# Optimization experiments

Measured on AMD Instinct MI355X. Metric: run time of the kernel, lower is better.

Reference implementation:

```python
import jax, jax.numpy as jnp
import numpy as np

B, I, H, O, T = 512, 512, 1024, 512, 128

def setup_inputs() -> dict:
    key = jax.random.key(0)
    ks = jax.random.split(key, 8)
    s_in = 1.0 / np.sqrt(I)
    s_h = 1.0 / np.sqrt(H)
    return {
        "x": jax.random.normal(ks[0], (B, I), dtype=jnp.float32),
        "h0": jnp.zeros((B, H), dtype=jnp.float32),
        "Wjx": jax.random.normal(ks[1], (H, I), dtype=jnp.float32) * s_in,
        "bjx": jnp.zeros((H,), dtype=jnp.float32),
        "Wjh": jax.random.normal(ks[2], (H, H), dtype=jnp.float32) * s_h,
        "bjh": jnp.zeros((H,), dtype=jnp.float32),
        "Wkx": jax.random.normal(ks[3], (H, I), dtype=jnp.float32) * s_in,
        "bkx": jnp.zeros((H,), dtype=jnp.float32),
        "Wkh": jax.random.normal(ks[4], (H, H), dtype=jnp.float32) * s_h,
        "bkh": jnp.zeros((H,), dtype=jnp.float32),
        "Wo": jax.random.normal(ks[5], (O, H), dtype=jnp.float32) * s_h,
        "bo": jnp.zeros((O,), dtype=jnp.float32),
        "seq_length": T,
    }

def reference(x, h0, Wjx, bjx, Wjh, bjh, Wkx, bkx, Wkh, bkh, Wo, bo, seq_length):
    # x is broadcast to every timestep (original repeats x along time).
    # Precompute the time-invariant input projections once; same math.
    jx = x @ Wjx.T + bjx  # [B,H]
    kx = x @ Wkx.T + bkx  # [B,H]

    def step(h, _):
        j = jax.nn.sigmoid(jx + h @ Wjh.T + bjh)
        k = jax.nn.sigmoid(kx + h @ Wkh.T + bkh)
        new_h = j * (1.0 - h) + (1.0 - k) * h
        out = new_h @ Wo.T + bo  # [B,O]
        return new_h, out

    h_final, outs = jax.lax.scan(step, h0, None, length=seq_length)
    outputs = jnp.transpose(outs, (1, 0, 2))  # [B,T,O]
    return outputs, h_final
```

## Files before the change

### kernel.cpp

```cpp
#include <hip/hip_runtime.h>
#include <hip/hip_bf16.h>
#include <hip/hip_cooperative_groups.h>

namespace cg = cooperative_groups;

constexpr int B = 512;
constexpr int I = 512;
constexpr int H = 1024;
constexpr int O = 512;

using short8 = __attribute__((ext_vector_type(8))) short;
using f32x4  = __attribute__((ext_vector_type(4))) float;
using bf16_t = __hip_bfloat16;

__device__ __forceinline__ short8 ldfrag(const bf16_t* p) {
    return *reinterpret_cast<const short8*>(p);
}
__device__ __forceinline__ float sigmoid_f(float z) {
    return 1.0f / (1.0f + __expf(-z));
}

__device__ __forceinline__ void group_wait(int* c, int target) {
    if (threadIdx.x == 0) {
        while (__hip_atomic_load(c, __ATOMIC_RELAXED, __HIP_MEMORY_SCOPE_AGENT) < target)
            __builtin_amdgcn_s_sleep(2);
    }
    __syncthreads();
    asm volatile("buffer_inv sc0" ::: "memory");
}
__device__ __forceinline__ void group_post(int* c) {
    __syncthreads();
    if (threadIdx.x == 0)
        __hip_atomic_fetch_add(c, 1, __ATOMIC_RELAXED, __HIP_MEMORY_SCOPE_AGENT);
}

__global__ __launch_bounds__(256, 2)
void flipflop_rnn_kernel(const float* __restrict__ x,  const float* __restrict__ h0,
                         const float* __restrict__ Wjx, const float* __restrict__ bjx,
                         const float* __restrict__ Wjh, const float* __restrict__ bjh,
                         const float* __restrict__ Wkx, const float* __restrict__ bkx,
                         const float* __restrict__ Wkh, const float* __restrict__ bkh,
                         const float* __restrict__ Wo,  const float* __restrict__ bo,
                         const int* __restrict__ seqlen,
                         float* __restrict__ out,
                         bf16_t* __restrict__ wjh_bf, bf16_t* __restrict__ wkh_bf,
                         bf16_t* __restrict__ wo_bf,  bf16_t* __restrict__ wjx_bf,
                         bf16_t* __restrict__ wkx_bf, bf16_t* __restrict__ x_bf,
                         bf16_t* __restrict__ hbf0,   bf16_t* __restrict__ hbf1,
                         int* __restrict__ cnt)
{
    __shared__ short lds_w[32768];

    const int T    = seqlen[0];
    const int tid  = threadIdx.x;
    const int g    = blockIdx.x;
    const int nthr = gridDim.x * blockDim.x;
    const int gtid = g * blockDim.x + tid;

    for (int idx = gtid; idx < H * H; idx += nthr) wjh_bf[idx] = __float2bfloat16(Wjh[idx]);
    for (int idx = gtid; idx < H * H; idx += nthr) wkh_bf[idx] = __float2bfloat16(Wkh[idx]);
    for (int idx = gtid; idx < O * H; idx += nthr) wo_bf[idx]  = __float2bfloat16(Wo[idx]);
    for (int idx = gtid; idx < H * I; idx += nthr) wjx_bf[idx] = __float2bfloat16(Wjx[idx]);
    for (int idx = gtid; idx < H * I; idx += nthr) wkx_bf[idx] = __float2bfloat16(Wkx[idx]);
    for (int idx = gtid; idx < B * I; idx += nthr) x_bf[idx]   = __float2bfloat16(x[idx]);
    if (gtid < 8 * 256) cnt[gtid] = 0;

    const int w     = tid >> 6;
    const int lane  = tid & 63;
    const int quad  = lane >> 4;
    const int lm    = lane & 15;
    const int iblk  = g & 7;
    const int lblk  = g >> 3;
    const int rbase = iblk * 64 + w * 16;
    const int n0    = lblk * 16;
    const bool has_out = (lblk < 32);
    const int no0   = lblk * 16;
    int* grp_cnt = cnt + iblk * 256;

    float hreg[4];
    #pragma unroll
    for (int r = 0; r < 4; ++r) {
        const int row = rbase + quad * 4 + r;
        const int col = n0 + lm;
        const float hv = h0[row * H + col];
        hreg[r] = hv;
        hbf0[row * H + col] = __float2bfloat16(hv);
    }

    cg::this_grid().sync();

    for (int c = tid; c < 4096; c += 256) {
        const int gate = c >> 11;
        const int cc   = c & 2047;
        const int kb   = cc >> 4;
        const int col  = cc & 15;
        const bf16_t* src = (gate ? wkh_bf : wjh_bf) + (n0 + col) * H + kb * 8;
        *reinterpret_cast<short8*>(&lds_w[c * 8]) = *reinterpret_cast<const short8*>(src);
    }
    __syncthreads();

    float jxr[4], kxr[4];
    {
        f32x4 aJ = {0.f, 0.f, 0.f, 0.f};
        f32x4 aK = {0.f, 0.f, 0.f, 0.f};
        const bf16_t* aP = x_bf   + (rbase + lm) * I + quad * 8;
        const bf16_t* jP = wjx_bf + (n0 + lm) * I + quad * 8;
        const bf16_t* kP = wkx_bf + (n0 + lm) * I + quad * 8;
        #pragma unroll 4
        for (int k0 = 0; k0 < I; k0 += 32) {
            short8 a = ldfrag(aP + k0);
            aJ = __builtin_amdgcn_mfma_f32_16x16x32_bf16(a, ldfrag(jP + k0), aJ, 0, 0, 0);
            aK = __builtin_amdgcn_mfma_f32_16x16x32_bf16(a, ldfrag(kP + k0), aK, 0, 0, 0);
        }
        const int col = n0 + lm;
        #pragma unroll
        for (int r = 0; r < 4; ++r) {
            jxr[r] = aJ[r] + bjx[col] + bjh[col];
            kxr[r] = aK[r] + bkx[col] + bkh[col];
        }
    }
    const float bo_v = has_out ? bo[no0 + lm] : 0.0f;

    for (int t = 0; t < T; ++t) {
        if (t > 0) group_wait(grp_cnt + t, 64);
        const bf16_t* hb  = (t & 1) ? hbf1 : hbf0;
        bf16_t*       hbn = (t & 1) ? hbf0 : hbf1;

        f32x4 accJ = {0.f, 0.f, 0.f, 0.f};
        f32x4 accK = {0.f, 0.f, 0.f, 0.f};
        f32x4 accO = {0.f, 0.f, 0.f, 0.f};

        const bf16_t* aP = hb    + (rbase + lm) * H + quad * 8;
        const bf16_t* oP = wo_bf + (no0 + lm) * H + quad * 8;
        const short*  jL = lds_w + quad * 128 + lm * 8;
        const short*  kL = jL + 16384;

        if (has_out) {
            #pragma unroll 4
            for (int k0 = 0; k0 < H; k0 += 32) {
                short8 a  = ldfrag(aP + k0);
                short8 bj = *reinterpret_cast<const short8*>(jL + (k0 >> 3) * 128);
                short8 bk = *reinterpret_cast<const short8*>(kL + (k0 >> 3) * 128);
                accJ = __builtin_amdgcn_mfma_f32_16x16x32_bf16(a, bj, accJ, 0, 0, 0);
                accK = __builtin_amdgcn_mfma_f32_16x16x32_bf16(a, bk, accK, 0, 0, 0);
                accO = __builtin_amdgcn_mfma_f32_16x16x32_bf16(a, ldfrag(oP + k0), accO, 0, 0, 0);
            }
        } else {
            #pragma unroll 4
            for (int k0 = 0; k0 < H; k0 += 32) {
                short8 a  = ldfrag(aP + k0);
                short8 bj = *reinterpret_cast<const short8*>(jL + (k0 >> 3) * 128);
                short8 bk = *reinterpret_cast<const short8*>(kL + (k0 >> 3) * 128);
                accJ = __builtin_amdgcn_mfma_f32_16x16x32_bf16(a, bj, accJ, 0, 0, 0);
                accK = __builtin_amdgcn_mfma_f32_16x16x32_bf16(a, bk, accK, 0, 0, 0);
            }
        }

        if (has_out && t > 0) {
            #pragma unroll
            for (int r = 0; r < 4; ++r) {
                const int row = rbase + quad * 4 + r;
                out[(row * T + (t - 1)) * O + no0 + lm] = accO[r] + bo_v;
            }
        }

        #pragma unroll
        for (int r = 0; r < 4; ++r) {
            const int row = rbase + quad * 4 + r;
            const int col = n0 + lm;
            const float jv = sigmoid_f(accJ[r] + jxr[r]);
            const float kv = sigmoid_f(accK[r] + kxr[r]);
            const float hv = hreg[r];
            const float hn = jv * (1.0f - hv) + (1.0f - kv) * hv;
            hreg[r] = hn;
            hbn[row * H + col] = __float2bfloat16(hn);
        }

        group_post(grp_cnt + t + 1);
    }

    group_wait(grp_cnt + T, 64);

    {
        const bf16_t* hb = (T & 1) ? hbf1 : hbf0;
        if (has_out) {
            f32x4 accO = {0.f, 0.f, 0.f, 0.f};
            const bf16_t* aP = hb    + (rbase + lm) * H + quad * 8;
            const bf16_t* oP = wo_bf + (no0 + lm) * H + quad * 8;
            #pragma unroll 4
            for (int k0 = 0; k0 < H; k0 += 32) {
                accO = __builtin_amdgcn_mfma_f32_16x16x32_bf16(ldfrag(aP + k0), ldfrag(oP + k0), accO, 0, 0, 0);
            }
            #pragma unroll
            for (int r = 0; r < 4; ++r) {
                const int row = rbase + quad * 4 + r;
                out[(row * T + (T - 1)) * O + no0 + lm] = accO[r] + bo_v;
            }
        }
        const int hfin = B * T * O;
        #pragma unroll
        for (int r = 0; r < 4; ++r) {
            const int row = rbase + quad * 4 + r;
            const int col = n0 + lm;
            out[hfin + row * H + col] = hreg[r];
        }
    }
}

extern "C" void kernel_launch(void* const* d_in, const int* in_sizes, int n_in,
                              void* d_out, int out_size, void* d_ws, size_t ws_size,
                              hipStream_t stream) {
    const float* x   = (const float*)d_in[0];
    const float* h0  = (const float*)d_in[1];
    const float* Wjx = (const float*)d_in[2];
    const float* bjx = (const float*)d_in[3];
    const float* Wjh = (const float*)d_in[4];
    const float* bjh = (const float*)d_in[5];
    const float* Wkx = (const float*)d_in[6];
    const float* bkx = (const float*)d_in[7];
    const float* Wkh = (const float*)d_in[8];
    const float* bkh = (const float*)d_in[9];
    const float* Wo  = (const float*)d_in[10];
    const float* bo  = (const float*)d_in[11];
    const int* seqlen = (const int*)d_in[12];
    float* out = (float*)d_out;

    char* ws = (char*)d_ws;
    bf16_t* wjh_bf = (bf16_t*)(ws + 0);
    bf16_t* wkh_bf = (bf16_t*)(ws + 2097152);
    bf16_t* wo_bf  = (bf16_t*)(ws + 4194304);
    bf16_t* wjx_bf = (bf16_t*)(ws + 5242880);
    bf16_t* wkx_bf = (bf16_t*)(ws + 6291456);
    bf16_t* x_bf   = (bf16_t*)(ws + 7340032);
    bf16_t* hbf0   = (bf16_t*)(ws + 7864320);
    bf16_t* hbf1   = (bf16_t*)(ws + 8912896);
    int*    cnt    = (int*)   (ws + 9961472);

    void* args[] = {
        &x, &h0, &Wjx, &bjx, &Wjh, &bjh, &Wkx, &bkx, &Wkh, &bkh, &Wo, &bo,
        &seqlen, &out,
        &wjh_bf, &wkh_bf, &wo_bf, &wjx_bf, &wkx_bf, &x_bf, &hbf0, &hbf1, &cnt
    };
    hipLaunchCooperativeKernel((const void*)flipflop_rnn_kernel,
                               dim3(512), dim3(256), args, 0, stream);
}
```

Before: 1.988 ms.

## Move output projection off the critical path with triple-buffered hidden state

The recurrent J/K matmul is split from the output projection. The output GEMM for the previous step now runs after the group post, so it overlaps with other groups' waits instead of delaying the barrier. A third hidden-state buffer is added so the buffer still being read for the output projection is not overwritten by the next step's writes. Both loops are fully unrolled with an 8-deep register prefetch of A and Wo fragments. This costs extra registers and re-reads the hidden state from global memory for the output projection.

After: 2.290 ms. 15.2% more time.

```diff
diff --git a/kernel.cpp b/kernel.cpp
--- a/kernel.cpp
+++ b/kernel.cpp
@@ -47,7 +47,7 @@
                          bf16_t* __restrict__ wo_bf,  bf16_t* __restrict__ wjx_bf,
                          bf16_t* __restrict__ wkx_bf, bf16_t* __restrict__ x_bf,
                          bf16_t* __restrict__ hbf0,   bf16_t* __restrict__ hbf1,
-                         int* __restrict__ cnt)
+                         bf16_t* __restrict__ hbf2,   int* __restrict__ cnt)
 {
     __shared__ short lds_w[32768];
 
@@ -121,47 +121,31 @@
     }
     const float bo_v = has_out ? bo[no0 + lm] : 0.0f;
 
+    constexpr int PF = 8;
+    bf16_t* hbufs[3] = {hbf0, hbf1, hbf2};
+
     for (int t = 0; t < T; ++t) {
         if (t > 0) group_wait(grp_cnt + t, 64);
-        const bf16_t* hb  = (t & 1) ? hbf1 : hbf0;
-        bf16_t*       hbn = (t & 1) ? hbf0 : hbf1;
+        const bf16_t* hb  = hbufs[t % 3];
+        bf16_t*       hbn = hbufs[(t + 1) % 3];
+
+        const bf16_t* aP = hb + (rbase + lm) * H + quad * 8;
+        const short*  jL = lds_w + quad * 128 + lm * 8;
+        const short*  kL = jL + 16384;
 
         f32x4 accJ = {0.f, 0.f, 0.f, 0.f};
         f32x4 accK = {0.f, 0.f, 0.f, 0.f};
-        f32x4 accO = {0.f, 0.f, 0.f, 0.f};
-
-        const bf16_t* aP = hb    + (rbase + lm) * H + quad * 8;
-        const bf16_t* oP = wo_bf + (no0 + lm) * H + quad * 8;
-        const short*  jL = lds_w + quad * 128 + lm * 8;
-        const short*  kL = jL + 16384;
-
-        if (has_out) {
-            #pragma unroll 4
-            for (int k0 = 0; k0 < H; k0 += 32) {
-                short8 a  = ldfrag(aP + k0);
-                short8 bj = *reinterpret_cast<const short8*>(jL + (k0 >> 3) * 128);
-                short8 bk = *reinterpret_cast<const short8*>(kL + (k0 >> 3) * 128);
-                accJ = __builtin_amdgcn_mfma_f32_16x16x32_bf16(a, bj, accJ, 0, 0, 0);
-                accK = __builtin_amdgcn_mfma_f32_16x16x32_bf16(a, bk, accK, 0, 0, 0);
-                accO = __builtin_amdgcn_mfma_f32_16x16x32_bf16(a, ldfrag(oP + k0), accO, 0, 0, 0);
-            }
-        } else {
-            #pragma unroll 4
-            for (int k0 = 0; k0 < H; k0 += 32) {
-                short8 a  = ldfrag(aP + k0);
-                short8 bj = *reinterpret_cast<const short8*>(jL + (k0 >> 3) * 128);
-                short8 bk = *reinterpret_cast<const short8*>(kL + (k0 >> 3) * 128);
-                accJ = __builtin_amdgcn_mfma_f32_16x16x32_bf16(a, bj, accJ, 0, 0, 0);
-                accK = __builtin_amdgcn_mfma_f32_16x16x32_bf16(a, bk, accK, 0, 0, 0);
-            }
-        }
-
-        if (has_out && t > 0) {
-            #pragma unroll
-            for (int r = 0; r < 4; ++r) {
-                const int row = rbase + quad * 4 + r;
-                out[(row * T + (t - 1)) * O + no0 + lm] = accO[r] + bo_v;
-            }
+        short8 af[PF];
+        #pragma unroll
+        for (int i = 0; i < PF; ++i) af[i] = ldfrag(aP + i * 32);
+        #pragma unroll
+        for (int k = 0; k < 32; ++k) {
+            short8 a = af[k & (PF - 1)];
+            if (k + PF < 32) af[k & (PF - 1)] = ldfrag(aP + (k + PF) * 32);
+            short8 bj = *reinterpret_cast<const short8*>(jL + k * 512);
+            short8 bk = *reinterpret_cast<const short8*>(kL + k * 512);
+            accJ = __builtin_amdgcn_mfma_f32_16x16x32_bf16(a, bj, accJ, 0, 0, 0);
+            accK = __builtin_amdgcn_mfma_f32_16x16x32_bf16(a, bk, accK, 0, 0, 0);
         }
 
         #pragma unroll
@@ -175,14 +159,36 @@
             hreg[r] = hn;
             hbn[row * H + col] = __float2bfloat16(hn);
         }
-
         group_post(grp_cnt + t + 1);
+
+        if (has_out && t > 0) {
+            f32x4 accO = {0.f, 0.f, 0.f, 0.f};
+            const bf16_t* oP = wo_bf + (no0 + lm) * H + quad * 8;
+            short8 aof[PF], wof[PF];
+            #pragma unroll
+            for (int i = 0; i < PF; ++i) { aof[i] = ldfrag(aP + i * 32); wof[i] = ldfrag(oP + i * 32); }
+            #pragma unroll
+            for (int k = 0; k < 32; ++k) {
+                short8 a  = aof[k & (PF - 1)];
+                short8 wo = wof[k & (PF - 1)];
+                if (k + PF < 32) {
+                    aof[k & (PF - 1)] = ldfrag(aP + (k + PF) * 32);
+                    wof[k & (PF - 1)] = ldfrag(oP + (k + PF) * 32);
+                }
+                accO = __builtin_amdgcn_mfma_f32_16x16x32_bf16(a, wo, accO, 0, 0, 0);
+            }
+            #pragma unroll
+            for (int r = 0; r < 4; ++r) {
+                const int row = rbase + quad * 4 + r;
+                out[(row * T + (t - 1)) * O + no0 + lm] = accO[r] + bo_v;
+            }
+        }
     }
 
     group_wait(grp_cnt + T, 64);
 
     {
-        const bf16_t* hb = (T & 1) ? hbf1 : hbf0;
+        const bf16_t* hb = hbufs[T % 3];
         if (has_out) {
             f32x4 accO = {0.f, 0.f, 0.f, 0.f};
             const bf16_t* aP = hb    + (rbase + lm) * H + quad * 8;
@@ -234,12 +240,13 @@
     bf16_t* x_bf   = (bf16_t*)(ws + 7340032);
     bf16_t* hbf0   = (bf16_t*)(ws + 7864320);
     bf16_t* hbf1   = (bf16_t*)(ws + 8912896);
-    int*    cnt    = (int*)   (ws + 9961472);
+    bf16_t* hbf2   = (bf16_t*)(ws + 9961472);
+    int*    cnt    = (int*)   (ws + 11010048);
 
     void* args[] = {
         &x, &h0, &Wjx, &bjx, &Wjh, &bjh, &Wkx, &bkx, &Wkh, &bkh, &Wo, &bo,
         &seqlen, &out,
-        &wjh_bf, &wkh_bf, &wo_bf, &wjx_bf, &wkx_bf, &x_bf, &hbf0, &hbf1, &cnt
+        &wjh_bf, &wkh_bf, &wo_bf, &wjx_bf, &wkx_bf, &x_bf, &hbf0, &hbf1, &hbf2, &cnt
     };
     hipLaunchCooperativeKernel((const void*)flipflop_rnn_kernel,
                                dim3(512), dim3(256), args, 0, stream);
```
